# Optimization experiments

Hardware: AMD Instinct MI355X
Metric: run time of the kernel (lower is better)

Reference implementation:

```python
import jax, jax.numpy as jnp
import numpy as np

NUM_HEADS = 16

def _rope_tables(seq_len, head_dim):
    # inv_freq over even indices; freqs = outer(t, inv_freq) -> [S, head_dim//2]
    inv_freq = 1.0 / (10000.0 ** (jnp.arange(0, head_dim, 2, dtype=jnp.float32) / head_dim))
    t = jnp.arange(seq_len, dtype=jnp.float32)
    freqs = t[:, None] * inv_freq[None, :]
    return jnp.cos(freqs), jnp.sin(freqs)  # each [S, head_dim//2]

def _apply_rope(x, cos, sin):
    # x: [B,H,S,hd]; cos/sin: [S, hd//2] broadcast to [1,1,S,hd//2]
    hd = x.shape[-1]
    x1, x2 = x[..., : hd // 2], x[..., hd // 2 :]
    c = cos[None, None]
    s = sin[None, None]
    return jnp.concatenate([x1 * c - x2 * s, x2 * c + x1 * s], axis=-1)

def setup_inputs() -> dict:
    key = jax.random.key(0)
    k1, k2, k3 = jax.random.split(key, 3)
    B, S, D = 2, 2048, 1024
    x = jax.random.normal(k1, (B, S, D), dtype=jnp.float32)
    w_qkv = jax.random.normal(k2, (3 * D, D), dtype=jnp.float32) * (2.0 / D) ** 0.5
    w_out = jax.random.normal(k3, (D, D), dtype=jnp.float32) * (2.0 / D) ** 0.5
    b_out = jnp.zeros((D,), dtype=jnp.float32)
    return {"x": x, "w_qkv": w_qkv, "w_out": w_out, "b_out": b_out}

def reference(x, w_qkv, w_out, b_out):
    B, S, D = x.shape
    H = NUM_HEADS
    hd = D // H
    scale = hd ** -0.5
    qkv = jnp.einsum("bsd,ed->bse", x, w_qkv)  # [B,S,3D]
    qkv = qkv.reshape(B, S, 3, H, hd).transpose(2, 0, 3, 1, 4)  # [3,B,H,S,hd]
    q, k, v = qkv[0], qkv[1], qkv[2]
    cos, sin = _rope_tables(S, hd)
    q = _apply_rope(q, cos, sin)
    k = _apply_rope(k, cos, sin)
    scores = jnp.einsum("bhqd,bhkd->bhqk", q, k) * scale  # [B,H,S,S]
    attn = jax.nn.softmax(scores, axis=-1)
    out = jnp.einsum("bhqk,bhkd->bhqd", attn, v)  # [B,H,S,hd]
    out = out.transpose(0, 2, 1, 3).reshape(B, S, D)
    return jnp.einsum("bsd,ed->bse", out, w_out) + b_out
```

## Files before the change

kernel.cpp:

```cpp
#include <hip/hip_runtime.h>
#include <hip/hip_bf16.h>
#include <math.h>

typedef __bf16 bf16;
typedef __attribute__((ext_vector_type(8))) __bf16 bf16x8;
typedef __attribute__((ext_vector_type(4))) __bf16 bf16x4;
typedef __attribute__((ext_vector_type(4))) float f32x4;
typedef __attribute__((ext_vector_type(16))) float f32x16;

#define MFMA16(a, b, c) __builtin_amdgcn_mfma_f32_16x16x32_bf16((a), (b), (c), 0, 0, 0)
#define MFMA32(a, b, c) __builtin_amdgcn_mfma_f32_32x32x16_bf16((a), (b), (c), 0, 0, 0)

__device__ __forceinline__ float fexp2(float x) { return __builtin_amdgcn_exp2f(x); }

__device__ __forceinline__ int swz(int row, int col) {
  return row * 64 + ((((col) >> 3) ^ (row & 7)) << 3) + (col & 7);
}

__device__ __forceinline__ void gl_lds16(const bf16* g, bf16* l) {
  __builtin_amdgcn_global_load_lds(
      (const __attribute__((address_space(1))) void*)g,
      (__attribute__((address_space(3))) void*)l, 16, 0, 0);
}

__global__ __launch_bounds__(256) void cvt_f32_bf16(const float* __restrict__ in,
                                                    bf16* __restrict__ out, int n4) {
  int i = blockIdx.x * 256 + threadIdx.x;
  if (i < n4) {
    float4 v = ((const float4*)in)[i];
    bf16x4 o = {(bf16)v.x, (bf16)v.y, (bf16)v.z, (bf16)v.w};
    ((bf16x4*)out)[i] = o;
  }
}

__global__ __launch_bounds__(256) void gemm_bt(const bf16* __restrict__ A,
                                               const bf16* __restrict__ Bm,
                                               float* __restrict__ Cf,
                                               const float* __restrict__ bias,
                                               int M, int N, int K) {
  __shared__ __align__(16) bf16 As[128 * 64];
  __shared__ __align__(16) bf16 Bs[128 * 64];
  const int t = threadIdx.x;
  const int w = t >> 6, l = t & 63;
  const int wr = w >> 1, wc = w & 1;
  const int lr = l & 15, lh = l >> 4;
  const int bm = blockIdx.x * 128, bn = blockIdx.y * 128;
  const int srow = l >> 3;
  const int schunk = (l & 7) ^ srow;

  f32x4 acc[4][4] = {};

  for (int k0 = 0; k0 < K; k0 += 64) {
    __syncthreads();
#pragma unroll
    for (int jj = 0; jj < 4; ++jj) {
      const int j = w + jj * 4;
      const int r = j * 8 + srow;
      gl_lds16(A + (size_t)(bm + r) * K + k0 + schunk * 8, As + j * 512);
      gl_lds16(Bm + (size_t)(bn + r) * K + k0 + schunk * 8, Bs + j * 512);
    }
    __syncthreads();
#pragma unroll
    for (int kk = 0; kk < 2; ++kk) {
      bf16x8 af[4], bfr[4];
#pragma unroll
      for (int mt = 0; mt < 4; ++mt)
        af[mt] = *(const bf16x8*)(As + swz(wr * 64 + mt * 16 + lr, kk * 32 + lh * 8));
#pragma unroll
      for (int nt = 0; nt < 4; ++nt)
        bfr[nt] = *(const bf16x8*)(Bs + swz(wc * 64 + nt * 16 + lr, kk * 32 + lh * 8));
#pragma unroll
      for (int mt = 0; mt < 4; ++mt)
#pragma unroll
        for (int nt = 0; nt < 4; ++nt)
          acc[mt][nt] = MFMA16(af[mt], bfr[nt], acc[mt][nt]);
    }
  }

#pragma unroll
  for (int mt = 0; mt < 4; ++mt)
#pragma unroll
    for (int nt = 0; nt < 4; ++nt)
#pragma unroll
      for (int r = 0; r < 4; ++r) {
        int m = bm + wr * 64 + mt * 16 + lh * 4 + r;
        int n = bn + wc * 64 + nt * 16 + lr;
        Cf[(size_t)m * N + n] = acc[mt][nt][r] + bias[n];
      }
}

__global__ __launch_bounds__(256) void gemm_qkv_rope(const bf16* __restrict__ A,
                                                     const bf16* __restrict__ Bm,
                                                     bf16* __restrict__ Qd,
                                                     bf16* __restrict__ Kd,
                                                     bf16* __restrict__ Vtg) {
  const int M = 4096, N = 3072, K = 1024;
  (void)M; (void)N;
  __shared__ __align__(16) bf16 As[128 * 64];
  __shared__ __align__(16) bf16 Bs[128 * 64];
  const int t = threadIdx.x;
  const int w = t >> 6, l = t & 63;
  const int wr = w >> 1, wc = w & 1;
  const int lr = l & 15, lh = l >> 4;
  const int bm = blockIdx.x * 128, bn = blockIdx.y * 128;
  const int srow = l >> 3;
  const int schunk = (l & 7) ^ srow;

  f32x4 acc[4][4] = {};

  for (int k0 = 0; k0 < K; k0 += 64) {
    __syncthreads();
#pragma unroll
    for (int jj = 0; jj < 4; ++jj) {
      const int j = w + jj * 4;
      const int r = j * 8 + srow;
      gl_lds16(A + (size_t)(bm + r) * K + k0 + schunk * 8, As + j * 512);
      gl_lds16(Bm + (size_t)(bn + r) * K + k0 + schunk * 8, Bs + j * 512);
    }
    __syncthreads();
#pragma unroll
    for (int kk = 0; kk < 2; ++kk) {
      bf16x8 af[4], bfr[4];
#pragma unroll
      for (int mt = 0; mt < 4; ++mt)
        af[mt] = *(const bf16x8*)(As + swz(wr * 64 + mt * 16 + lr, kk * 32 + lh * 8));
#pragma unroll
      for (int nt = 0; nt < 4; ++nt)
        bfr[nt] = *(const bf16x8*)(Bs + swz(wc * 64 + nt * 16 + lr, kk * 32 + lh * 8));
#pragma unroll
      for (int mt = 0; mt < 4; ++mt)
#pragma unroll
        for (int nt = 0; nt < 4; ++nt)
          acc[mt][nt] = MFMA16(af[mt], bfr[nt], acc[mt][nt]);
    }
  }

  const int b = bm >> 11;
  const int sbase = (bm & 2047) + wr * 64 + lh * 4;
  const int sec = bn >> 10;
  const int h = ((bn & 1023) + wc * 64) >> 6;
  const int bh = b * 16 + h;

  if (sec < 2) {
    bf16* dst = (sec == 0 ? Qd : Kd) + (size_t)bh * 2048 * 64;
    const float QSs = sec == 0 ? 0.18033688011112042f : 1.0f;
#pragma unroll
    for (int nt = 0; nt < 2; ++nt) {
      const int j = nt * 16 + lr;
      const float ifr = fexp2((float)j * -0.4152410118609203f) *
                        0.15915494309189535f;
#pragma unroll
      for (int mt = 0; mt < 4; ++mt) {
#pragma unroll
        for (int r = 0; r < 4; ++r) {
          const int s = sbase + mt * 16 + r;
          float rev = (float)s * ifr;
          rev -= floorf(rev);
          float c  = __builtin_amdgcn_cosf(rev);
          float sn = __builtin_amdgcn_sinf(rev);
          float x1 = acc[mt][nt][r], x2 = acc[mt][nt + 2][r];
          dst[(size_t)s * 64 + j]      = (bf16)((x1 * c - x2 * sn) * QSs);
          dst[(size_t)s * 64 + j + 32] = (bf16)((x2 * c + x1 * sn) * QSs);
        }
      }
    }
  } else {
    bf16* dst = Vtg + (size_t)bh * 131072;
#pragma unroll
    for (int nt = 0; nt < 4; ++nt) {
      const int d = nt * 16 + lr;
#pragma unroll
      for (int mt = 0; mt < 4; ++mt) {
        const int g = sbase + mt * 16;
        const int gp = (g & ~12) | ((g & 4) << 1) | ((g & 8) >> 1);
        bf16x4 v4 = {(bf16)acc[mt][nt][0], (bf16)acc[mt][nt][1],
                     (bf16)acc[mt][nt][2], (bf16)acc[mt][nt][3]};
        *(bf16x4*)(dst + (size_t)d * 2048 + gp) = v4;
      }
    }
  }
}

__global__ __launch_bounds__(256) void attn_fwd(const bf16* __restrict__ Qg,
                                                const bf16* __restrict__ Kg,
                                                const bf16* __restrict__ Vtg,
                                                bf16* __restrict__ Og) {
  __shared__ __align__(16) bf16 Ks[32 * 128];
  __shared__ __align__(16) bf16 Vt[32 * 128];
  const int bh = blockIdx.x, qt = blockIdx.y;
  const int t = threadIdx.x, wv = t >> 6, l = t & 63;
  const int lq = l & 31, hi = l >> 5;
  const bf16* Qb  = Qg  + (size_t)bh * 2048 * 64;
  const bf16* Kb  = Kg  + (size_t)bh * 2048 * 64;
  const bf16* Vtb = Vtg + (size_t)bh * 131072;
  const int q = qt * 128 + wv * 32 + lq;

  bf16x8 qf[4];
#pragma unroll
  for (int s = 0; s < 4; ++s)
    qf[s] = *(const bf16x8*)(Qb + (size_t)q * 64 + s * 16 + hi * 8);

  f32x16 o0 = {}, o1 = {};
  float lsum = 0.f;

  const int r0 = t >> 2, c0 = (t & 3) * 16;
  const int srow = r0 & 31;
  const int L0 = ((r0 >> 5) << 3) + (c0 >> 3);
  const int off0 = srow * 128 + (((L0)     ^ (r0 & 15)) << 3);
  const int off1 = srow * 128 + (((L0 + 1) ^ (r0 & 15)) << 3);

  bf16x8 kreg0 = *(const bf16x8*)(Kb + (size_t)r0 * 64 + c0);
  bf16x8 kreg1 = *(const bf16x8*)(Kb + (size_t)r0 * 64 + c0 + 8);
  bf16x8 vreg0 = *(const bf16x8*)(Vtb + (size_t)r0 * 2048 + c0);
  bf16x8 vreg1 = *(const bf16x8*)(Vtb + (size_t)r0 * 2048 + c0 + 8);

  for (int tt = 0; tt < 32; ++tt) {
    __syncthreads();
    *(bf16x8*)(Ks + off0) = kreg0;
    *(bf16x8*)(Ks + off1) = kreg1;
    *(bf16x8*)(Vt + off0) = vreg0;
    *(bf16x8*)(Vt + off1) = vreg1;
    __syncthreads();

    if (tt + 1 < 32) {
      const int KV2 = (tt + 1) * 64;
      kreg0 = *(const bf16x8*)(Kb + (size_t)(KV2 + r0) * 64 + c0);
      kreg1 = *(const bf16x8*)(Kb + (size_t)(KV2 + r0) * 64 + c0 + 8);
      vreg0 = *(const bf16x8*)(Vtb + (size_t)r0 * 2048 + KV2 + c0);
      vreg1 = *(const bf16x8*)(Vtb + (size_t)r0 * 2048 + KV2 + c0 + 8);
    }

    f32x16 p0 = {}, p1 = {};
#pragma unroll
    for (int s = 0; s < 4; ++s) {
      bf16x8 ka0 = *(const bf16x8*)(Ks + lq * 128 + (((2 * s + hi) ^ (lq & 15)) << 3));
      bf16x8 ka1 = *(const bf16x8*)(Ks + lq * 128 + (((8 + 2 * s + hi) ^ (lq & 15)) << 3));
      p0 = MFMA32(ka0, qf[s], p0);
      p1 = MFMA32(ka1, qf[s], p1);
    }

#pragma unroll
    for (int j = 0; j < 16; ++j) {
      p0[j] = fexp2(p0[j]);
      p1[j] = fexp2(p1[j]);
    }
    float l0 = 0.f, l1 = 0.f, l2 = 0.f, l3 = 0.f;
#pragma unroll
    for (int j = 0; j < 16; j += 4) {
      l0 += p0[j]; l1 += p0[j + 1]; l2 += p0[j + 2]; l3 += p0[j + 3];
      l0 += p1[j]; l1 += p1[j + 1]; l2 += p1[j + 2]; l3 += p1[j + 3];
    }
    lsum += (l0 + l1) + (l2 + l3);

#pragma unroll
    for (int s = 0; s < 4; ++s) {
      bf16x8 pb;
#pragma unroll
      for (int e = 0; e < 8; ++e) {
        float pv = (s == 0) ? p0[e] : (s == 1) ? p0[8 + e]
                 : (s == 2) ? p1[e] : p1[8 + e];
        pb[e] = (bf16)pv;
      }
      bf16x8 va0 = *(const bf16x8*)(Vt + lq * 128 + (((2 * s + hi) ^ (lq & 15)) << 3));
      bf16x8 va1 = *(const bf16x8*)(Vt + lq * 128 + (((8 + 2 * s + hi) ^ (lq & 15)) << 3));
      o0 = MFMA32(va0, pb, o0);
      o1 = MFMA32(va1, pb, o1);
    }
  }

  float inv = 1.0f / (lsum + __shfl_xor(lsum, 32));
  const int b = bh >> 4, h = bh & 15;
  bf16* orow = Og + (size_t)(b * 2048 + q) * 1024 + h * 64;
#pragma unroll
  for (int dblk = 0; dblk < 2; ++dblk) {
#pragma unroll
    for (int J = 0; J < 4; ++J) {
      float e0 = (dblk ? o1[4 * J] : o0[4 * J]) * inv;
      float e1 = (dblk ? o1[4 * J + 1] : o0[4 * J + 1]) * inv;
      float e2 = (dblk ? o1[4 * J + 2] : o0[4 * J + 2]) * inv;
      float e3 = (dblk ? o1[4 * J + 3] : o0[4 * J + 3]) * inv;
      bf16x4 wv2 = {(bf16)e0, (bf16)e1, (bf16)e2, (bf16)e3};
      *(bf16x4*)(orow + dblk * 32 + 8 * J + 4 * hi) = wv2;
    }
  }
}

extern "C" void kernel_launch(void* const* d_in, const int* in_sizes, int n_in,
                              void* d_out, int out_size, void* d_ws, size_t ws_size,
                              hipStream_t stream) {
  const float* x     = (const float*)d_in[0];
  const float* w_qkv = (const float*)d_in[1];
  const float* w_out = (const float*)d_in[2];
  const float* b_out = (const float*)d_in[3];
  float* out = (float*)d_out;
  char* ws = (char*)d_ws;
  const size_t MB = 1024 * 1024;

  bf16* xb    = (bf16*)(ws);
  bf16* wqkvb = (bf16*)(ws + 8 * MB);
  bf16* woutb = (bf16*)(ws + 14 * MB);
  bf16* Qd    = (bf16*)(ws + 40 * MB);
  bf16* Kd    = (bf16*)(ws + 48 * MB);
  bf16* Vtg   = (bf16*)(ws + 56 * MB);
  bf16* attnb = xb;

  cvt_f32_bf16<<<4096, 256, 0, stream>>>(x, xb, 1048576);
  cvt_f32_bf16<<<3072, 256, 0, stream>>>(w_qkv, wqkvb, 786432);
  cvt_f32_bf16<<<1024, 256, 0, stream>>>(w_out, woutb, 262144);

  gemm_qkv_rope<<<dim3(32, 24), 256, 0, stream>>>(xb, wqkvb, Qd, Kd, Vtg);
  attn_fwd<<<dim3(32, 16), 256, 0, stream>>>(Qd, Kd, Vtg, attnb);
  gemm_bt<<<dim3(32, 8), 256, 0, stream>>>(attnb, woutb, out, b_out,
                                           4096, 1024, 1024);
}
```

Baseline: 127.4 us.

## Merge conversion kernels, compute softmax row sums via MFMA, add setprio around MFMAs

```diff
diff --git a/kernel.cpp b/kernel.cpp
--- a/kernel.cpp
+++ b/kernel.cpp
@@ -23,14 +23,22 @@
       (__attribute__((address_space(3))) void*)l, 16, 0, 0);
 }
 
-__global__ __launch_bounds__(256) void cvt_f32_bf16(const float* __restrict__ in,
-                                                    bf16* __restrict__ out, int n4) {
+__global__ __launch_bounds__(256) void cvt_all(const float* __restrict__ x,
+                                               const float* __restrict__ wq,
+                                               const float* __restrict__ wo,
+                                               bf16* __restrict__ xb,
+                                               bf16* __restrict__ wqb,
+                                               bf16* __restrict__ wob) {
   int i = blockIdx.x * 256 + threadIdx.x;
-  if (i < n4) {
-    float4 v = ((const float4*)in)[i];
-    bf16x4 o = {(bf16)v.x, (bf16)v.y, (bf16)v.z, (bf16)v.w};
-    ((bf16x4*)out)[i] = o;
-  }
+  const float* src;
+  bf16* dst;
+  int off;
+  if (i < 1048576)       { src = x;  dst = xb;  off = i; }
+  else if (i < 1835008)  { src = wq; dst = wqb; off = i - 1048576; }
+  else                   { src = wo; dst = wob; off = i - 1835008; }
+  float4 v = ((const float4*)src)[off];
+  bf16x4 o = {(bf16)v.x, (bf16)v.y, (bf16)v.z, (bf16)v.w};
+  ((bf16x4*)dst)[off] = o;
 }
 
 __global__ __launch_bounds__(256) void gemm_bt(const bf16* __restrict__ A,
@@ -94,8 +102,7 @@
                                                      bf16* __restrict__ Qd,
                                                      bf16* __restrict__ Kd,
                                                      bf16* __restrict__ Vtg) {
-  const int M = 4096, N = 3072, K = 1024;
-  (void)M; (void)N;
+  const int K = 1024;
   __shared__ __align__(16) bf16 As[128 * 64];
   __shared__ __align__(16) bf16 Bs[128 * 64];
   const int t = threadIdx.x;
@@ -200,8 +207,12 @@
   for (int s = 0; s < 4; ++s)
     qf[s] = *(const bf16x8*)(Qb + (size_t)q * 64 + s * 16 + hi * 8);
 
+  bf16x8 onesf;
+#pragma unroll
+  for (int e = 0; e < 8; ++e) onesf[e] = (bf16)1.0f;
+
   f32x16 o0 = {}, o1 = {};
-  float lsum = 0.f;
+  f32x16 lacc = {};
 
   const int r0 = t >> 2, c0 = (t & 3) * 16;
   const int srow = r0 & 31;
@@ -231,6 +242,7 @@
     }
 
     f32x16 p0 = {}, p1 = {};
+    __builtin_amdgcn_s_setprio(1);
 #pragma unroll
     for (int s = 0; s < 4; ++s) {
       bf16x8 ka0 = *(const bf16x8*)(Ks + lq * 128 + (((2 * s + hi) ^ (lq & 15)) << 3));
@@ -238,20 +250,15 @@
       p0 = MFMA32(ka0, qf[s], p0);
       p1 = MFMA32(ka1, qf[s], p1);
     }
+    __builtin_amdgcn_s_setprio(0);
 
 #pragma unroll
     for (int j = 0; j < 16; ++j) {
       p0[j] = fexp2(p0[j]);
       p1[j] = fexp2(p1[j]);
     }
-    float l0 = 0.f, l1 = 0.f, l2 = 0.f, l3 = 0.f;
-#pragma unroll
-    for (int j = 0; j < 16; j += 4) {
-      l0 += p0[j]; l1 += p0[j + 1]; l2 += p0[j + 2]; l3 += p0[j + 3];
-      l0 += p1[j]; l1 += p1[j + 1]; l2 += p1[j + 2]; l3 += p1[j + 3];
-    }
-    lsum += (l0 + l1) + (l2 + l3);
-
+
+    __builtin_amdgcn_s_setprio(1);
 #pragma unroll
     for (int s = 0; s < 4; ++s) {
       bf16x8 pb;
@@ -265,10 +272,12 @@
       bf16x8 va1 = *(const bf16x8*)(Vt + lq * 128 + (((8 + 2 * s + hi) ^ (lq & 15)) << 3));
       o0 = MFMA32(va0, pb, o0);
       o1 = MFMA32(va1, pb, o1);
-    }
-  }
-
-  float inv = 1.0f / (lsum + __shfl_xor(lsum, 32));
+      lacc = MFMA32(onesf, pb, lacc);
+    }
+    __builtin_amdgcn_s_setprio(0);
+  }
+
+  float inv = 1.0f / lacc[0];
   const int b = bh >> 4, h = bh & 15;
   bf16* orow = Og + (size_t)(b * 2048 + q) * 1024 + h * 64;
 #pragma unroll
@@ -304,9 +313,7 @@
   bf16* Vtg   = (bf16*)(ws + 56 * MB);
   bf16* attnb = xb;
 
-  cvt_f32_bf16<<<4096, 256, 0, stream>>>(x, xb, 1048576);
-  cvt_f32_bf16<<<3072, 256, 0, stream>>>(w_qkv, wqkvb, 786432);
-  cvt_f32_bf16<<<1024, 256, 0, stream>>>(w_out, woutb, 262144);
+  cvt_all<<<8192, 256, 0, stream>>>(x, w_qkv, w_out, xb, wqkvb, woutb);
 
   gemm_qkv_rope<<<dim3(32, 24), 256, 0, stream>>>(xb, wqkvb, Qd, Kd, Vtg);
   attn_fwd<<<dim3(32, 16), 256, 0, stream>>>(Qd, Kd, Vtg, attnb);
```

Measured after the change: 123.6 us. 1.03x faster.
